# Optimization experiments

Hardware: AMD Instinct MI355X
Metric: run time of the kernel (lower is better)

## Reference

```python
import jax, jax.numpy as jnp
import numpy as np

N_AGENTS = 512
HID = 256
OBS = 128


def setup_inputs() -> dict:
    key = jax.random.key(0)
    ks = jax.random.split(key, 10)
    s = 0.02  # weight init scale
    f32 = jnp.float32
    return {
        "inputs": jax.random.normal(ks[0], (N_AGENTS, OBS), f32),
        "fc1_w": jax.random.normal(ks[1], (HID, OBS), f32) * s,
        "fc1_b": jnp.zeros((HID,), f32),
        "in_proj_w": jax.random.normal(ks[2], (3 * HID, HID), f32) * s,
        "in_proj_b": jnp.zeros((3 * HID,), f32),
        "out_proj_w": jax.random.normal(ks[3], (HID, HID), f32) * s,
        "out_proj_b": jnp.zeros((HID,), f32),
        "fc2_w": jax.random.normal(ks[4], (HID, 2 * HID), f32) * s,
        "fc2_b": jnp.zeros((HID,), f32),
        "fc3_w": jax.random.normal(ks[5], (2, HID), f32) * s,
        "fc3_b": jnp.zeros((2,), f32),
        "vfc2_w": jax.random.normal(ks[6], (HID, HID * N_AGENTS), f32) * s,
        "vfc2_b": jnp.zeros((HID,), f32),
        "vfc3_w": jax.random.normal(ks[7], (1, HID), f32) * s,
        "vfc3_b": jnp.zeros((1,), f32),
    }


def reference(inputs, fc1_w, fc1_b, in_proj_w, in_proj_b, out_proj_w, out_proj_b,
              fc2_w, fc2_b, fc3_w, fc3_b, vfc2_w, vfc2_b, vfc3_w, vfc3_b):
    n = inputs.shape[0]
    d = fc1_w.shape[0]
    # per-agent embed
    hid = jax.nn.relu(inputs @ fc1_w.T + fc1_b)                 # [n, d]
    # single-head self-attention (torch MultiheadAttention, 1 head)
    qkv = hid @ in_proj_w.T + in_proj_b                         # [n, 3d]
    q, k, v = jnp.split(qkv, 3, axis=-1)
    scores = (q @ k.T) / jnp.sqrt(jnp.asarray(d, hid.dtype))    # [n, n]
    attn = jax.nn.softmax(scores, axis=-1)
    h = (attn @ v) @ out_proj_w.T + out_proj_b                  # [n, d]
    # all-pairs edge features restricted to strict upper triangle
    iu0, iu1 = jnp.triu_indices(n, 1)                           # P = n(n-1)/2
    pairs = jnp.concatenate([h[iu0], h[iu1]], axis=1)           # [P, 2d]
    x = jax.nn.relu(pairs @ fc2_w.T + fc2_b)                    # [P, d]
    action_out = jax.nn.softmax(x @ fc3_w.T + fc3_b, axis=-1)   # [P, 2]
    # value head over flattened node embeddings
    vh = jax.nn.relu(hid.reshape(1, -1) @ vfc2_w.T + vfc2_b)    # [1, d]
    value = vh @ vfc3_w.T + vfc3_b                              # [1, 1]
    value = jnp.broadcast_to(value, (action_out.shape[0], 1))   # [P, 1]
    return jnp.concatenate([action_out, value], axis=1)         # [P, 3]
```

## Files before the change

kernel.cpp:

```cpp
#include <hip/hip_runtime.h>
#include <math.h>

#define N_AG   512
#define HIDD   256
#define OBSD   128

__device__ __forceinline__ float dot4(float4 a, float4 b){
    return a.x*b.x + a.y*b.y + a.z*b.z + a.w*b.w;
}

__global__ __launch_bounds__(256) void k_fc1(const float* __restrict__ in,
        const float* __restrict__ w, const float* __restrict__ b,
        float* __restrict__ hid){
    __shared__ float lin[8*OBSD];
    int at = blockIdx.y, ot = blockIdx.x, t = threadIdx.x;
    ((float4*)lin)[t] = ((const float4*)(in + at*8*OBSD))[t];
    __syncthreads();
    int ol = t & 63, g = t >> 6;
    int o = ot*64 + ol;
    const float4* w4 = (const float4*)(w + o*OBSD);
    const float4* la = (const float4*)(lin + (g*2)*OBSD);
    const float4* lb = (const float4*)(lin + (g*2+1)*OBSD);
    float acc0 = 0.f, acc1 = 0.f;
    #pragma unroll
    for (int c = 0; c < OBSD/4; ++c){
        float4 wv = w4[c];
        acc0 += dot4(la[c], wv);
        acc1 += dot4(lb[c], wv);
    }
    float bb = b[o];
    int a0 = at*8 + g*2;
    hid[a0*HIDD + o]     = fmaxf(acc0 + bb, 0.f);
    hid[(a0+1)*HIDD + o] = fmaxf(acc1 + bb, 0.f);
}

__global__ __launch_bounds__(256) void k_qkv(const float* __restrict__ hid,
        const float* __restrict__ w, const float* __restrict__ b,
        float* __restrict__ qkv){
    __shared__ float lin[8*HIDD];
    int at = blockIdx.y, ot = blockIdx.x, t = threadIdx.x;
    const float4* in4 = (const float4*)(hid + at*8*HIDD);
    ((float4*)lin)[t]       = in4[t];
    ((float4*)lin)[t + 256] = in4[t + 256];
    __syncthreads();
    int ol = t & 63, g = t >> 6;
    int o = ot*64 + ol;
    const float4* w4 = (const float4*)(w + o*HIDD);
    const float4* la = (const float4*)(lin + (g*2)*HIDD);
    const float4* lb = (const float4*)(lin + (g*2+1)*HIDD);
    float acc0 = 0.f, acc1 = 0.f;
    #pragma unroll 16
    for (int c = 0; c < HIDD/4; ++c){
        float4 wv = w4[c];
        acc0 += dot4(la[c], wv);
        acc1 += dot4(lb[c], wv);
    }
    float bb = b[o];
    int a0 = at*8 + g*2;
    qkv[a0*768 + o]     = acc0 + bb;
    qkv[(a0+1)*768 + o] = acc1 + bb;
}

__global__ __launch_bounds__(256) void k_attn(const float* __restrict__ qkv,
        const float* __restrict__ ow, const float* __restrict__ ob,
        float* __restrict__ hout){
    __shared__ float q2[2*HIDD];
    __shared__ float sc[2*512];
    __shared__ float av[2*HIDD];
    __shared__ float red[16];
    int r0 = blockIdx.x*2, t = threadIdx.x;
    if (t < 128){
        int r = t >> 6, c4 = t & 63;
        ((float4*)q2)[r*64 + c4] = ((const float4*)(qkv + (r0+r)*768))[c4];
    }
    __syncthreads();
    #pragma unroll
    for (int jj = 0; jj < 2; ++jj){
        int j = t + jj*256;
        const float4* k4 = (const float4*)(qkv + j*768 + HIDD);
        const float4* qa = (const float4*)q2;
        const float4* qb = (const float4*)(q2 + HIDD);
        float a0 = 0.f, a1 = 0.f;
        #pragma unroll 16
        for (int c = 0; c < HIDD/4; ++c){
            float4 kv = k4[c];
            a0 += dot4(qa[c], kv);
            a1 += dot4(qb[c], kv);
        }
        sc[j]       = a0 * 0.0625f;
        sc[512 + j] = a1 * 0.0625f;
    }
    __syncthreads();
    int lane = t & 63, wid = t >> 6;
    float s00 = sc[t], s01 = sc[t+256], s10 = sc[512+t], s11 = sc[512+t+256];
    float m0 = fmaxf(s00, s01), m1 = fmaxf(s10, s11);
    for (int off = 32; off; off >>= 1){
        m0 = fmaxf(m0, __shfl_xor(m0, off));
        m1 = fmaxf(m1, __shfl_xor(m1, off));
    }
    if (lane == 0){ red[wid] = m0; red[4+wid] = m1; }
    __syncthreads();
    m0 = fmaxf(fmaxf(red[0],red[1]), fmaxf(red[2],red[3]));
    m1 = fmaxf(fmaxf(red[4],red[5]), fmaxf(red[6],red[7]));
    float e00 = expf(s00-m0), e01 = expf(s01-m0), e10 = expf(s10-m1), e11 = expf(s11-m1);
    float t0 = e00+e01, t1 = e10+e11;
    for (int off = 32; off; off >>= 1){ t0 += __shfl_xor(t0, off); t1 += __shfl_xor(t1, off); }
    if (lane == 0){ red[8+wid] = t0; red[12+wid] = t1; }
    __syncthreads();
    float inv0 = 1.f/(red[8]+red[9]+red[10]+red[11]);
    float inv1 = 1.f/(red[12]+red[13]+red[14]+red[15]);
    sc[t] = e00*inv0; sc[t+256] = e01*inv0;
    sc[512+t] = e10*inv1; sc[512+t+256] = e11*inv1;
    __syncthreads();
    {
        float acc0 = 0.f, acc1 = 0.f;
        for (int j = 0; j < 512; ++j){
            float vv = qkv[j*768 + 512 + t];
            acc0 += sc[j]*vv;
            acc1 += sc[512+j]*vv;
        }
        av[t] = acc0; av[HIDD+t] = acc1;
    }
    __syncthreads();
    {
        const float4* w4 = (const float4*)(ow + t*HIDD);
        const float4* a4 = (const float4*)av;
        const float4* b4 = (const float4*)(av + HIDD);
        float h0 = 0.f, h1 = 0.f;
        #pragma unroll 16
        for (int c = 0; c < HIDD/4; ++c){
            float4 wv = w4[c];
            h0 += dot4(a4[c], wv);
            h1 += dot4(b4[c], wv);
        }
        float bb = ob[t];
        hout[r0*HIDD + t]     = h0 + bb;
        hout[(r0+1)*HIDD + t] = h1 + bb;
    }
}

__global__ __launch_bounds__(256) void k_ab(const float* __restrict__ hin,
        const float* __restrict__ w, const float* __restrict__ b,
        float* __restrict__ A, float* __restrict__ B){
    __shared__ float lin[8*HIDD];
    int at = blockIdx.y, ot = blockIdx.x, t = threadIdx.x;
    const float4* in4 = (const float4*)(hin + at*8*HIDD);
    ((float4*)lin)[t]       = in4[t];
    ((float4*)lin)[t + 256] = in4[t + 256];
    __syncthreads();
    int ol = t & 63, g = t >> 6;
    int o2 = ot*64 + ol;
    bool isA = o2 < HIDD;
    int o = isA ? o2 : o2 - HIDD;
    const float4* w4 = (const float4*)(w + o*512 + (isA ? 0 : HIDD));
    const float4* la = (const float4*)(lin + (g*2)*HIDD);
    const float4* lb = (const float4*)(lin + (g*2+1)*HIDD);
    float acc0 = 0.f, acc1 = 0.f;
    #pragma unroll 16
    for (int c = 0; c < HIDD/4; ++c){
        float4 wv = w4[c];
        acc0 += dot4(la[c], wv);
        acc1 += dot4(lb[c], wv);
    }
    int a0 = at*8 + g*2;
    float* dst = isA ? A : B;
    float bb = isA ? b[o] : 0.f;
    dst[a0*HIDD + o]     = acc0 + bb;
    dst[(a0+1)*HIDD + o] = acc1 + bb;
}

__global__ __launch_bounds__(256) void k_vpart(const float* __restrict__ hid,
        const float* __restrict__ vw, float* __restrict__ partial){
    int chunk = blockIdx.x, o = blockIdx.y, t = threadIdx.x;
    const float4* h4 = (const float4*)hid;
    const float4* w4 = (const float4*)vw;
    long base  = (long)chunk*4096;
    long wbase = (long)o*32768 + base;
    float acc = 0.f;
    #pragma unroll 4
    for (int it = 0; it < 16; ++it){
        acc += dot4(h4[base + it*256 + t], w4[wbase + it*256 + t]);
    }
    for (int off = 32; off; off >>= 1) acc += __shfl_xor(acc, off);
    __shared__ float red[4];
    int lane = t & 63, wid = t >> 6;
    if (lane == 0) red[wid] = acc;
    __syncthreads();
    if (t == 0) partial[o*8 + chunk] = red[0]+red[1]+red[2]+red[3];
}

__global__ __launch_bounds__(256) void k_value(const float* __restrict__ partial,
        const float* __restrict__ vb, const float* __restrict__ v3w,
        const float* __restrict__ v3b, float* __restrict__ value){
    int t = threadIdx.x;
    float s = vb[t];
    #pragma unroll
    for (int c = 0; c < 8; ++c) s += partial[t*8 + c];
    s = fmaxf(s, 0.f);
    float p = s * v3w[t];
    for (int off = 32; off; off >>= 1) p += __shfl_xor(p, off);
    __shared__ float red[4];
    int lane = t & 63, wid = t >> 6;
    if (lane == 0) red[wid] = p;
    __syncthreads();
    if (t == 0) value[0] = red[0]+red[1]+red[2]+red[3] + v3b[0];
}

__global__ __launch_bounds__(256) void k_pairs(const float* __restrict__ A,
        const float* __restrict__ B, const float* __restrict__ w3,
        const float* __restrict__ b3, const float* __restrict__ value,
        float* __restrict__ out){
    int ti = blockIdx.x, tj = blockIdx.y;
    if (tj < ti) return;
    __shared__ float la[16*260], lb[16*260], lw[256];
    int t = threadIdx.x;
    #pragma unroll
    for (int l = 0; l < 4; ++l){
        int idx = l*256 + t;
        int r = idx >> 6, c4 = idx & 63;
        ((float4*)la)[r*65 + c4] = ((const float4*)A)[(ti*16 + r)*64 + c4];
        ((float4*)lb)[r*65 + c4] = ((const float4*)B)[(tj*16 + r)*64 + c4];
    }
    lw[t] = w3[t] - w3[256 + t];
    __syncthreads();
    float val = value[0];
    float bd  = b3[0] - b3[1];
    int il = t >> 4, jl = t & 15;
    int i = ti*16 + il, j = tj*16 + jl;
    if (j > i){
        const float4* a4 = (const float4*)(la + il*260);
        const float4* b4 = (const float4*)(lb + jl*260);
        const float4* w4 = (const float4*)lw;
        float acc = 0.f;
        #pragma unroll 8
        for (int c = 0; c < 64; ++c){
            float4 aa = a4[c], bb = b4[c], wv = w4[c];
            acc += fmaxf(aa.x + bb.x, 0.f)*wv.x
                 + fmaxf(aa.y + bb.y, 0.f)*wv.y
                 + fmaxf(aa.z + bb.z, 0.f)*wv.z
                 + fmaxf(aa.w + bb.w, 0.f)*wv.w;
        }
        float z = acc + bd;
        float o0 = 1.f/(1.f + expf(-z));
        int p = i*511 - (i*(i-1))/2 + (j - i - 1);
        out[3*p]   = o0;
        out[3*p+1] = 1.f - o0;
        out[3*p+2] = val;
    }
}

extern "C" void kernel_launch(void* const* d_in, const int* in_sizes, int n_in,
                              void* d_out, int out_size, void* d_ws, size_t ws_size,
                              hipStream_t stream){
    const float* inputs = (const float*)d_in[0];
    const float* fc1_w  = (const float*)d_in[1];
    const float* fc1_b  = (const float*)d_in[2];
    const float* inp_w  = (const float*)d_in[3];
    const float* inp_b  = (const float*)d_in[4];
    const float* outp_w = (const float*)d_in[5];
    const float* outp_b = (const float*)d_in[6];
    const float* fc2_w  = (const float*)d_in[7];
    const float* fc2_b  = (const float*)d_in[8];
    const float* fc3_w  = (const float*)d_in[9];
    const float* fc3_b  = (const float*)d_in[10];
    const float* vfc2_w = (const float*)d_in[11];
    const float* vfc2_b = (const float*)d_in[12];
    const float* vfc3_w = (const float*)d_in[13];
    const float* vfc3_b = (const float*)d_in[14];
    float* out = (float*)d_out;
    float* ws  = (float*)d_ws;
    float* hid     = ws;
    float* qkv     = ws + 131072;
    float* h       = ws + 524288;
    float* A       = ws + 655360;
    float* B       = ws + 786432;
    float* partial = ws + 917504;
    float* value   = ws + 919552;

    k_fc1  <<<dim3(4, 64),  256, 0, stream>>>(inputs, fc1_w, fc1_b, hid);
    k_qkv  <<<dim3(12, 64), 256, 0, stream>>>(hid, inp_w, inp_b, qkv);
    k_attn <<<dim3(256),    256, 0, stream>>>(qkv, outp_w, outp_b, h);
    k_ab   <<<dim3(8, 64),  256, 0, stream>>>(h, fc2_w, fc2_b, A, B);
    k_vpart<<<dim3(8, 256), 256, 0, stream>>>(hid, vfc2_w, partial);
    k_value<<<1,            256, 0, stream>>>(partial, vfc2_b, vfc3_w, vfc3_b, value);
    k_pairs<<<dim3(32, 32), 256, 0, stream>>>(A, B, fc3_w, fc3_b, value, out);
}
```

Baseline: 335.3 us.

## Fuse kernels into four launches and split dot-product accumulators

Merges fc1 and the QKV projection into one embed kernel, and runs the value-head partial reduction as extra blocks inside the attention launch. The final value reduction is folded into the A/B projection kernel. Attention now handles one row per block, so there are twice as many blocks, and all dot products use four independent accumulators to shorten the dependency chain. This cuts the launch count from seven to four and overlaps the independent value-head work with attention. In exchange, attention reuses each loaded K/V row across fewer query rows, and the embed kernel has only 128 blocks, each doing more serial work.

New measurement: 435.1 us. 1.3x slower.

```diff
diff --git a/kernel.cpp b/kernel.cpp
--- a/kernel.cpp
+++ b/kernel.cpp
@@ -5,145 +5,138 @@
 #define HIDD   256
 #define OBSD   128
 
-__device__ __forceinline__ float dot4(float4 a, float4 b){
-    return a.x*b.x + a.y*b.y + a.z*b.z + a.w*b.w;
-}
-
-__global__ __launch_bounds__(256) void k_fc1(const float* __restrict__ in,
-        const float* __restrict__ w, const float* __restrict__ b,
-        float* __restrict__ hid){
-    __shared__ float lin[8*OBSD];
-    int at = blockIdx.y, ot = blockIdx.x, t = threadIdx.x;
-    ((float4*)lin)[t] = ((const float4*)(in + at*8*OBSD))[t];
+__device__ __forceinline__ void fma4(float4& acc, float4 a, float4 b){
+    acc.x += a.x*b.x; acc.y += a.y*b.y; acc.z += a.z*b.z; acc.w += a.w*b.w;
+}
+__device__ __forceinline__ float hsum(float4 a){ return (a.x+a.y)+(a.z+a.w); }
+
+__global__ __launch_bounds__(256) void k_embed(const float* __restrict__ in,
+        const float* __restrict__ w1, const float* __restrict__ b1,
+        const float* __restrict__ wq, const float* __restrict__ bq,
+        float* __restrict__ hid, float* __restrict__ qkv){
+    __shared__ float lin[4*OBSD];
+    __shared__ float lh[4*HIDD];
+    int at = blockIdx.x, t = threadIdx.x;
+    if (t < 128) ((float4*)lin)[t] = ((const float4*)(in + at*4*OBSD))[t];
     __syncthreads();
     int ol = t & 63, g = t >> 6;
-    int o = ot*64 + ol;
-    const float4* w4 = (const float4*)(w + o*OBSD);
-    const float4* la = (const float4*)(lin + (g*2)*OBSD);
-    const float4* lb = (const float4*)(lin + (g*2+1)*OBSD);
-    float acc0 = 0.f, acc1 = 0.f;
+    const float4* x4 = (const float4*)(lin + g*OBSD);
     #pragma unroll
-    for (int c = 0; c < OBSD/4; ++c){
-        float4 wv = w4[c];
-        acc0 += dot4(la[c], wv);
-        acc1 += dot4(lb[c], wv);
-    }
-    float bb = b[o];
-    int a0 = at*8 + g*2;
-    hid[a0*HIDD + o]     = fmaxf(acc0 + bb, 0.f);
-    hid[(a0+1)*HIDD + o] = fmaxf(acc1 + bb, 0.f);
-}
-
-__global__ __launch_bounds__(256) void k_qkv(const float* __restrict__ hid,
-        const float* __restrict__ w, const float* __restrict__ b,
-        float* __restrict__ qkv){
-    __shared__ float lin[8*HIDD];
-    int at = blockIdx.y, ot = blockIdx.x, t = threadIdx.x;
-    const float4* in4 = (const float4*)(hid + at*8*HIDD);
-    ((float4*)lin)[t]       = in4[t];
-    ((float4*)lin)[t + 256] = in4[t + 256];
-    __syncthreads();
-    int ol = t & 63, g = t >> 6;
-    int o = ot*64 + ol;
-    const float4* w4 = (const float4*)(w + o*HIDD);
-    const float4* la = (const float4*)(lin + (g*2)*HIDD);
-    const float4* lb = (const float4*)(lin + (g*2+1)*HIDD);
-    float acc0 = 0.f, acc1 = 0.f;
-    #pragma unroll 16
-    for (int c = 0; c < HIDD/4; ++c){
-        float4 wv = w4[c];
-        acc0 += dot4(la[c], wv);
-        acc1 += dot4(lb[c], wv);
-    }
-    float bb = b[o];
-    int a0 = at*8 + g*2;
-    qkv[a0*768 + o]     = acc0 + bb;
-    qkv[(a0+1)*768 + o] = acc1 + bb;
-}
-
-__global__ __launch_bounds__(256) void k_attn(const float* __restrict__ qkv,
+    for (int ot = 0; ot < 4; ++ot){
+        int o = ot*64 + ol;
+        const float4* w4 = (const float4*)(w1 + o*OBSD);
+        float4 acc = {0,0,0,0};
+        #pragma unroll
+        for (int c = 0; c < OBSD/4; ++c) fma4(acc, x4[c], w4[c]);
+        float h = fmaxf(hsum(acc) + b1[o], 0.f);
+        lh[g*HIDD + o] = h;
+        hid[(at*4+g)*HIDD + o] = h;
+    }
+    __syncthreads();
+    const float4* h4 = (const float4*)(lh + g*HIDD);
+    #pragma unroll 2
+    for (int ot = 0; ot < 12; ++ot){
+        int o = ot*64 + ol;
+        const float4* w4 = (const float4*)(wq + o*HIDD);
+        float4 acc = {0,0,0,0};
+        #pragma unroll 16
+        for (int c = 0; c < HIDD/4; ++c) fma4(acc, h4[c], w4[c]);
+        qkv[(at*4+g)*768 + o] = hsum(acc) + bq[o];
+    }
+}
+
+__global__ __launch_bounds__(256) void k_attn_vpart(const float* __restrict__ qkv,
         const float* __restrict__ ow, const float* __restrict__ ob,
-        float* __restrict__ hout){
-    __shared__ float q2[2*HIDD];
-    __shared__ float sc[2*512];
-    __shared__ float av[2*HIDD];
-    __shared__ float red[16];
-    int r0 = blockIdx.x*2, t = threadIdx.x;
-    if (t < 128){
-        int r = t >> 6, c4 = t & 63;
-        ((float4*)q2)[r*64 + c4] = ((const float4*)(qkv + (r0+r)*768))[c4];
-    }
-    __syncthreads();
+        const float* __restrict__ hid, const float* __restrict__ vw,
+        float* __restrict__ hout, float* __restrict__ partial){
+    int t = threadIdx.x;
+    if (blockIdx.x >= N_AG){
+        int id = blockIdx.x - N_AG;
+        int chunk = id & 7, o = id >> 3;
+        const float4* h4 = (const float4*)hid;
+        const float4* w4 = (const float4*)vw;
+        long base  = (long)chunk*4096;
+        long wbase = (long)o*32768 + base;
+        float4 acc4 = {0,0,0,0};
+        #pragma unroll 4
+        for (int it = 0; it < 16; ++it)
+            fma4(acc4, h4[base + it*256 + t], w4[wbase + it*256 + t]);
+        float acc = hsum(acc4);
+        for (int off = 32; off; off >>= 1) acc += __shfl_xor(acc, off);
+        __shared__ float redv[4];
+        int lane = t & 63, wid = t >> 6;
+        if (lane == 0) redv[wid] = acc;
+        __syncthreads();
+        if (t == 0) partial[o*8 + chunk] = redv[0]+redv[1]+redv[2]+redv[3];
+        return;
+    }
+    int r = blockIdx.x;
+    __shared__ float q[HIDD];
+    __shared__ float sc[512];
+    __shared__ float av[HIDD];
+    __shared__ float red2[8];
+    if (t < 64) ((float4*)q)[t] = ((const float4*)(qkv + r*768))[t];
+    __syncthreads();
+    const float4* q4 = (const float4*)q;
     #pragma unroll
     for (int jj = 0; jj < 2; ++jj){
         int j = t + jj*256;
         const float4* k4 = (const float4*)(qkv + j*768 + HIDD);
-        const float4* qa = (const float4*)q2;
-        const float4* qb = (const float4*)(q2 + HIDD);
-        float a0 = 0.f, a1 = 0.f;
+        float4 acc = {0,0,0,0};
         #pragma unroll 16
-        for (int c = 0; c < HIDD/4; ++c){
-            float4 kv = k4[c];
-            a0 += dot4(qa[c], kv);
-            a1 += dot4(qb[c], kv);
-        }
-        sc[j]       = a0 * 0.0625f;
-        sc[512 + j] = a1 * 0.0625f;
+        for (int c = 0; c < HIDD/4; ++c) fma4(acc, q4[c], k4[c]);
+        sc[j] = hsum(acc) * 0.0625f;
     }
     __syncthreads();
     int lane = t & 63, wid = t >> 6;
-    float s00 = sc[t], s01 = sc[t+256], s10 = sc[512+t], s11 = sc[512+t+256];
-    float m0 = fmaxf(s00, s01), m1 = fmaxf(s10, s11);
-    for (int off = 32; off; off >>= 1){
-        m0 = fmaxf(m0, __shfl_xor(m0, off));
-        m1 = fmaxf(m1, __shfl_xor(m1, off));
-    }
-    if (lane == 0){ red[wid] = m0; red[4+wid] = m1; }
-    __syncthreads();
-    m0 = fmaxf(fmaxf(red[0],red[1]), fmaxf(red[2],red[3]));
-    m1 = fmaxf(fmaxf(red[4],red[5]), fmaxf(red[6],red[7]));
-    float e00 = expf(s00-m0), e01 = expf(s01-m0), e10 = expf(s10-m1), e11 = expf(s11-m1);
-    float t0 = e00+e01, t1 = e10+e11;
-    for (int off = 32; off; off >>= 1){ t0 += __shfl_xor(t0, off); t1 += __shfl_xor(t1, off); }
-    if (lane == 0){ red[8+wid] = t0; red[12+wid] = t1; }
-    __syncthreads();
-    float inv0 = 1.f/(red[8]+red[9]+red[10]+red[11]);
-    float inv1 = 1.f/(red[12]+red[13]+red[14]+red[15]);
-    sc[t] = e00*inv0; sc[t+256] = e01*inv0;
-    sc[512+t] = e10*inv1; sc[512+t+256] = e11*inv1;
-    __syncthreads();
-    {
-        float acc0 = 0.f, acc1 = 0.f;
-        for (int j = 0; j < 512; ++j){
-            float vv = qkv[j*768 + 512 + t];
-            acc0 += sc[j]*vv;
-            acc1 += sc[512+j]*vv;
-        }
-        av[t] = acc0; av[HIDD+t] = acc1;
-    }
-    __syncthreads();
-    {
-        const float4* w4 = (const float4*)(ow + t*HIDD);
-        const float4* a4 = (const float4*)av;
-        const float4* b4 = (const float4*)(av + HIDD);
-        float h0 = 0.f, h1 = 0.f;
-        #pragma unroll 16
-        for (int c = 0; c < HIDD/4; ++c){
-            float4 wv = w4[c];
-            h0 += dot4(a4[c], wv);
-            h1 += dot4(b4[c], wv);
-        }
-        float bb = ob[t];
-        hout[r0*HIDD + t]     = h0 + bb;
-        hout[(r0+1)*HIDD + t] = h1 + bb;
-    }
-}
-
-__global__ __launch_bounds__(256) void k_ab(const float* __restrict__ hin,
-        const float* __restrict__ w, const float* __restrict__ b,
-        float* __restrict__ A, float* __restrict__ B){
+    float s0 = sc[t], s1 = sc[t+256];
+    float m = fmaxf(s0, s1);
+    for (int off = 32; off; off >>= 1) m = fmaxf(m, __shfl_xor(m, off));
+    if (lane == 0) red2[wid] = m;
+    __syncthreads();
+    m = fmaxf(fmaxf(red2[0],red2[1]), fmaxf(red2[2],red2[3]));
+    float e0 = expf(s0-m), e1 = expf(s1-m);
+    float s = e0 + e1;
+    for (int off = 32; off; off >>= 1) s += __shfl_xor(s, off);
+    if (lane == 0) red2[4+wid] = s;
+    __syncthreads();
+    float inv = 1.f/(red2[4]+red2[5]+red2[6]+red2[7]);
+    sc[t] = e0*inv; sc[t+256] = e1*inv;
+    __syncthreads();
+    float acc = 0.f;
+    #pragma unroll 8
+    for (int j = 0; j < 512; ++j) acc += sc[j]*qkv[j*768 + 512 + t];
+    av[t] = acc;
+    __syncthreads();
+    const float4* a4 = (const float4*)av;
+    const float4* w4 = (const float4*)(ow + t*HIDD);
+    float4 acc4 = {0,0,0,0};
+    #pragma unroll 16
+    for (int c = 0; c < HIDD/4; ++c) fma4(acc4, a4[c], w4[c]);
+    hout[r*HIDD + t] = hsum(acc4) + ob[t];
+}
+
+__global__ __launch_bounds__(256) void k_ab_value(const float* __restrict__ hin,
+        const float* __restrict__ w2, const float* __restrict__ b2,
+        const float* __restrict__ partial, const float* __restrict__ vb,
+        const float* __restrict__ v3w, const float* __restrict__ v3b,
+        float* __restrict__ A, float* __restrict__ B, float* __restrict__ value){
+    int t = threadIdx.x;
+    if (blockIdx.x == 512){
+        float s = vb[t];
+        #pragma unroll
+        for (int c = 0; c < 8; ++c) s += partial[t*8 + c];
+        s = fmaxf(s, 0.f) * v3w[t];
+        for (int off = 32; off; off >>= 1) s += __shfl_xor(s, off);
+        __shared__ float redv[4];
+        int lane = t & 63, wid = t >> 6;
+        if (lane == 0) redv[wid] = s;
+        __syncthreads();
+        if (t == 0) value[0] = redv[0]+redv[1]+redv[2]+redv[3] + v3b[0];
+        return;
+    }
     __shared__ float lin[8*HIDD];
-    int at = blockIdx.y, ot = blockIdx.x, t = threadIdx.x;
+    int id = blockIdx.x, at = id >> 3, ot = id & 7;
     const float4* in4 = (const float4*)(hin + at*8*HIDD);
     ((float4*)lin)[t]       = in4[t];
     ((float4*)lin)[t + 256] = in4[t + 256];
@@ -152,58 +145,21 @@
     int o2 = ot*64 + ol;
     bool isA = o2 < HIDD;
     int o = isA ? o2 : o2 - HIDD;
-    const float4* w4 = (const float4*)(w + o*512 + (isA ? 0 : HIDD));
+    const float4* w4 = (const float4*)(w2 + o*512 + (isA ? 0 : HIDD));
     const float4* la = (const float4*)(lin + (g*2)*HIDD);
     const float4* lb = (const float4*)(lin + (g*2+1)*HIDD);
-    float acc0 = 0.f, acc1 = 0.f;
+    float4 acc0 = {0,0,0,0}, acc1 = {0,0,0,0};
     #pragma unroll 16
     for (int c = 0; c < HIDD/4; ++c){
         float4 wv = w4[c];
-        acc0 += dot4(la[c], wv);
-        acc1 += dot4(lb[c], wv);
+        fma4(acc0, la[c], wv);
+        fma4(acc1, lb[c], wv);
     }
     int a0 = at*8 + g*2;
     float* dst = isA ? A : B;
-    float bb = isA ? b[o] : 0.f;
-    dst[a0*HIDD + o]     = acc0 + bb;
-    dst[(a0+1)*HIDD + o] = acc1 + bb;
-}
-
-__global__ __launch_bounds__(256) void k_vpart(const float* __restrict__ hid,
-        const float* __restrict__ vw, float* __restrict__ partial){
-    int chunk = blockIdx.x, o = blockIdx.y, t = threadIdx.x;
-    const float4* h4 = (const float4*)hid;
-    const float4* w4 = (const float4*)vw;
-    long base  = (long)chunk*4096;
-    long wbase = (long)o*32768 + base;
-    float acc = 0.f;
-    #pragma unroll 4
-    for (int it = 0; it < 16; ++it){
-        acc += dot4(h4[base + it*256 + t], w4[wbase + it*256 + t]);
-    }
-    for (int off = 32; off; off >>= 1) acc += __shfl_xor(acc, off);
-    __shared__ float red[4];
-    int lane = t & 63, wid = t >> 6;
-    if (lane == 0) red[wid] = acc;
-    __syncthreads();
-    if (t == 0) partial[o*8 + chunk] = red[0]+red[1]+red[2]+red[3];
-}
-
-__global__ __launch_bounds__(256) void k_value(const float* __restrict__ partial,
-        const float* __restrict__ vb, const float* __restrict__ v3w,
-        const float* __restrict__ v3b, float* __restrict__ value){
-    int t = threadIdx.x;
-    float s = vb[t];
-    #pragma unroll
-    for (int c = 0; c < 8; ++c) s += partial[t*8 + c];
-    s = fmaxf(s, 0.f);
-    float p = s * v3w[t];
-    for (int off = 32; off; off >>= 1) p += __shfl_xor(p, off);
-    __shared__ float red[4];
-    int lane = t & 63, wid = t >> 6;
-    if (lane == 0) red[wid] = p;
-    __syncthreads();
-    if (t == 0) value[0] = red[0]+red[1]+red[2]+red[3] + v3b[0];
+    float bb = isA ? b2[o] : 0.f;
+    dst[a0*HIDD + o]     = hsum(acc0) + bb;
+    dst[(a0+1)*HIDD + o] = hsum(acc1) + bb;
 }
 
 __global__ __launch_bounds__(256) void k_pairs(const float* __restrict__ A,
@@ -231,16 +187,16 @@
         const float4* a4 = (const float4*)(la + il*260);
         const float4* b4 = (const float4*)(lb + jl*260);
         const float4* w4 = (const float4*)lw;
-        float acc = 0.f;
+        float4 acc = {0,0,0,0};
         #pragma unroll 8
         for (int c = 0; c < 64; ++c){
             float4 aa = a4[c], bb = b4[c], wv = w4[c];
-            acc += fmaxf(aa.x + bb.x, 0.f)*wv.x
-                 + fmaxf(aa.y + bb.y, 0.f)*wv.y
-                 + fmaxf(aa.z + bb.z, 0.f)*wv.z
-                 + fmaxf(aa.w + bb.w, 0.f)*wv.w;
+            acc.x += fmaxf(aa.x + bb.x, 0.f)*wv.x;
+            acc.y += fmaxf(aa.y + bb.y, 0.f)*wv.y;
+            acc.z += fmaxf(aa.z + bb.z, 0.f)*wv.z;
+            acc.w += fmaxf(aa.w + bb.w, 0.f)*wv.w;
         }
-        float z = acc + bd;
+        float z = hsum(acc) + bd;
         float o0 = 1.f/(1.f + expf(-z));
         int p = i*511 - (i*(i-1))/2 + (j - i - 1);
         out[3*p]   = o0;
@@ -277,11 +233,8 @@
     float* partial = ws + 917504;
     float* value   = ws + 919552;
 
-    k_fc1  <<<dim3(4, 64),  256, 0, stream>>>(inputs, fc1_w, fc1_b, hid);
-    k_qkv  <<<dim3(12, 64), 256, 0, stream>>>(hid, inp_w, inp_b, qkv);
-    k_attn <<<dim3(256),    256, 0, stream>>>(qkv, outp_w, outp_b, h);
-    k_ab   <<<dim3(8, 64),  256, 0, stream>>>(h, fc2_w, fc2_b, A, B);
-    k_vpart<<<dim3(8, 256), 256, 0, stream>>>(hid, vfc2_w, partial);
-    k_value<<<1,            256, 0, stream>>>(partial, vfc2_b, vfc3_w, vfc3_b, value);
-    k_pairs<<<dim3(32, 32), 256, 0, stream>>>(A, B, fc3_w, fc3_b, value, out);
-}
+    k_embed     <<<dim3(128),       256, 0, stream>>>(inputs, fc1_w, fc1_b, inp_w, inp_b, hid, qkv);
+    k_attn_vpart<<<dim3(2560),      256, 0, stream>>>(qkv, outp_w, outp_b, hid, vfc2_w, h, partial);
+    k_ab_value  <<<dim3(513),       256, 0, stream>>>(h, fc2_w, fc2_b, partial, vfc2_b, vfc3_w, vfc3_b, A, B, value);
+    k_pairs     <<<dim3(32, 32),    256, 0, stream>>>(A, B, fc3_w, fc3_b, value, out);
+}
```

## Merge value-head kernels into attention and fc2 launches; use vector accumulators

Applied to the files above, without the earlier changes.

The value-head partial reduction now runs as extra blocks inside the attention kernel, and the final value reduction runs as an extra block of the fc2 A/B kernel. This cuts the launch count from seven to five and lets the memory-bound value-head weight stream overlap with the attention blocks. Dot-product loops also switch to four independent float4 accumulators to break the serial FMA dependency chain, and the attention V loop gets an unroll pragma. The cost is more register pressure and slightly different floating-point summation order.

Result: faster. 314.2 us (-6.3%).

```diff
diff --git a/kernel.cpp b/kernel.cpp
--- a/kernel.cpp
+++ b/kernel.cpp
@@ -5,9 +5,10 @@
 #define HIDD   256
 #define OBSD   128
 
-__device__ __forceinline__ float dot4(float4 a, float4 b){
-    return a.x*b.x + a.y*b.y + a.z*b.z + a.w*b.w;
-}
+__device__ __forceinline__ void fma4(float4& acc, float4 a, float4 b){
+    acc.x += a.x*b.x; acc.y += a.y*b.y; acc.z += a.z*b.z; acc.w += a.w*b.w;
+}
+__device__ __forceinline__ float hsum(float4 a){ return (a.x+a.y)+(a.z+a.w); }
 
 __global__ __launch_bounds__(256) void k_fc1(const float* __restrict__ in,
         const float* __restrict__ w, const float* __restrict__ b,
@@ -21,17 +22,17 @@
     const float4* w4 = (const float4*)(w + o*OBSD);
     const float4* la = (const float4*)(lin + (g*2)*OBSD);
     const float4* lb = (const float4*)(lin + (g*2+1)*OBSD);
-    float acc0 = 0.f, acc1 = 0.f;
+    float4 a0 = {0,0,0,0}, a1 = {0,0,0,0};
     #pragma unroll
     for (int c = 0; c < OBSD/4; ++c){
         float4 wv = w4[c];
-        acc0 += dot4(la[c], wv);
-        acc1 += dot4(lb[c], wv);
+        fma4(a0, la[c], wv);
+        fma4(a1, lb[c], wv);
     }
     float bb = b[o];
-    int a0 = at*8 + g*2;
-    hid[a0*HIDD + o]     = fmaxf(acc0 + bb, 0.f);
-    hid[(a0+1)*HIDD + o] = fmaxf(acc1 + bb, 0.f);
+    int ag = at*8 + g*2;
+    hid[ag*HIDD + o]     = fmaxf(hsum(a0) + bb, 0.f);
+    hid[(ag+1)*HIDD + o] = fmaxf(hsum(a1) + bb, 0.f);
 }
 
 __global__ __launch_bounds__(256) void k_qkv(const float* __restrict__ hid,
@@ -48,47 +49,69 @@
     const float4* w4 = (const float4*)(w + o*HIDD);
     const float4* la = (const float4*)(lin + (g*2)*HIDD);
     const float4* lb = (const float4*)(lin + (g*2+1)*HIDD);
-    float acc0 = 0.f, acc1 = 0.f;
+    float4 a0 = {0,0,0,0}, a1 = {0,0,0,0};
     #pragma unroll 16
     for (int c = 0; c < HIDD/4; ++c){
         float4 wv = w4[c];
-        acc0 += dot4(la[c], wv);
-        acc1 += dot4(lb[c], wv);
+        fma4(a0, la[c], wv);
+        fma4(a1, lb[c], wv);
     }
     float bb = b[o];
-    int a0 = at*8 + g*2;
-    qkv[a0*768 + o]     = acc0 + bb;
-    qkv[(a0+1)*768 + o] = acc1 + bb;
-}
-
-__global__ __launch_bounds__(256) void k_attn(const float* __restrict__ qkv,
+    int ag = at*8 + g*2;
+    qkv[ag*768 + o]     = hsum(a0) + bb;
+    qkv[(ag+1)*768 + o] = hsum(a1) + bb;
+}
+
+__global__ __launch_bounds__(256) void k_attn_vpart(const float* __restrict__ qkv,
         const float* __restrict__ ow, const float* __restrict__ ob,
-        float* __restrict__ hout){
+        const float* __restrict__ hid, const float* __restrict__ vw,
+        float* __restrict__ hout, float* __restrict__ partial){
+    int t = threadIdx.x;
+    if (blockIdx.x >= 256){
+        int id = blockIdx.x - 256;
+        int chunk = id & 7, o = id >> 3;
+        const float4* h4 = (const float4*)hid;
+        const float4* w4 = (const float4*)vw;
+        long base  = (long)chunk*4096;
+        long wbase = (long)o*32768 + base;
+        float4 acc4 = {0,0,0,0};
+        #pragma unroll 4
+        for (int it = 0; it < 16; ++it)
+            fma4(acc4, h4[base + it*256 + t], w4[wbase + it*256 + t]);
+        float acc = hsum(acc4);
+        for (int off = 32; off; off >>= 1) acc += __shfl_xor(acc, off);
+        __shared__ float redv[4];
+        int lane = t & 63, wid = t >> 6;
+        if (lane == 0) redv[wid] = acc;
+        __syncthreads();
+        if (t == 0) partial[o*8 + chunk] = redv[0]+redv[1]+redv[2]+redv[3];
+        return;
+    }
+    int r0 = blockIdx.x*2;
     __shared__ float q2[2*HIDD];
     __shared__ float sc[2*512];
     __shared__ float av[2*HIDD];
     __shared__ float red[16];
-    int r0 = blockIdx.x*2, t = threadIdx.x;
     if (t < 128){
         int r = t >> 6, c4 = t & 63;
         ((float4*)q2)[r*64 + c4] = ((const float4*)(qkv + (r0+r)*768))[c4];
     }
     __syncthreads();
+    const float4* qa = (const float4*)q2;
+    const float4* qb = (const float4*)(q2 + HIDD);
     #pragma unroll
     for (int jj = 0; jj < 2; ++jj){
         int j = t + jj*256;
         const float4* k4 = (const float4*)(qkv + j*768 + HIDD);
-        const float4* qa = (const float4*)q2;
-        const float4* qb = (const float4*)(q2 + HIDD);
-        float a0 = 0.f, a1 = 0.f;
+        float4 acc0 = {0,0,0,0}, acc1 = {0,0,0,0};
         #pragma unroll 16
         for (int c = 0; c < HIDD/4; ++c){
             float4 kv = k4[c];
-            a0 += dot4(qa[c], kv);
-            a1 += dot4(qb[c], kv);
-        }
-        sc[j]       = a0 * 0.0625f;
-        sc[512 + j] = a1 * 0.0625f;
+            fma4(acc0, qa[c], kv);
+            fma4(acc1, qb[c], kv);
+        }
+        sc[j]       = hsum(acc0) * 0.0625f;
+        sc[512 + j] = hsum(acc1) * 0.0625f;
     }
     __syncthreads();
     int lane = t & 63, wid = t >> 6;
@@ -114,6 +137,7 @@
     __syncthreads();
     {
         float acc0 = 0.f, acc1 = 0.f;
+        #pragma unroll 8
         for (int j = 0; j < 512; ++j){
             float vv = qkv[j*768 + 512 + t];
             acc0 += sc[j]*vv;
@@ -126,24 +150,40 @@
         const float4* w4 = (const float4*)(ow + t*HIDD);
         const float4* a4 = (const float4*)av;
         const float4* b4 = (const float4*)(av + HIDD);
-        float h0 = 0.f, h1 = 0.f;
+        float4 h0 = {0,0,0,0}, h1 = {0,0,0,0};
         #pragma unroll 16
         for (int c = 0; c < HIDD/4; ++c){
             float4 wv = w4[c];
-            h0 += dot4(a4[c], wv);
-            h1 += dot4(b4[c], wv);
+            fma4(h0, a4[c], wv);
+            fma4(h1, b4[c], wv);
         }
         float bb = ob[t];
-        hout[r0*HIDD + t]     = h0 + bb;
-        hout[(r0+1)*HIDD + t] = h1 + bb;
-    }
-}
-
-__global__ __launch_bounds__(256) void k_ab(const float* __restrict__ hin,
-        const float* __restrict__ w, const float* __restrict__ b,
-        float* __restrict__ A, float* __restrict__ B){
+        hout[r0*HIDD + t]     = hsum(h0) + bb;
+        hout[(r0+1)*HIDD + t] = hsum(h1) + bb;
+    }
+}
+
+__global__ __launch_bounds__(256) void k_ab_value(const float* __restrict__ hin,
+        const float* __restrict__ w2, const float* __restrict__ b2,
+        const float* __restrict__ partial, const float* __restrict__ vb,
+        const float* __restrict__ v3w, const float* __restrict__ v3b,
+        float* __restrict__ A, float* __restrict__ B, float* __restrict__ value){
+    int t = threadIdx.x;
+    if (blockIdx.x == 512){
+        float s = vb[t];
+        #pragma unroll
+        for (int c = 0; c < 8; ++c) s += partial[t*8 + c];
+        s = fmaxf(s, 0.f) * v3w[t];
+        for (int off = 32; off; off >>= 1) s += __shfl_xor(s, off);
+        __shared__ float redv[4];
+        int lane = t & 63, wid = t >> 6;
+        if (lane == 0) redv[wid] = s;
+        __syncthreads();
+        if (t == 0) value[0] = redv[0]+redv[1]+redv[2]+redv[3] + v3b[0];
+        return;
+    }
     __shared__ float lin[8*HIDD];
-    int at = blockIdx.y, ot = blockIdx.x, t = threadIdx.x;
+    int id = blockIdx.x, at = id >> 3, ot = id & 7;
     const float4* in4 = (const float4*)(hin + at*8*HIDD);
     ((float4*)lin)[t]       = in4[t];
     ((float4*)lin)[t + 256] = in4[t + 256];
@@ -152,58 +192,21 @@
     int o2 = ot*64 + ol;
     bool isA = o2 < HIDD;
     int o = isA ? o2 : o2 - HIDD;
-    const float4* w4 = (const float4*)(w + o*512 + (isA ? 0 : HIDD));
+    const float4* w4 = (const float4*)(w2 + o*512 + (isA ? 0 : HIDD));
     const float4* la = (const float4*)(lin + (g*2)*HIDD);
     const float4* lb = (const float4*)(lin + (g*2+1)*HIDD);
-    float acc0 = 0.f, acc1 = 0.f;
+    float4 acc0 = {0,0,0,0}, acc1 = {0,0,0,0};
     #pragma unroll 16
     for (int c = 0; c < HIDD/4; ++c){
         float4 wv = w4[c];
-        acc0 += dot4(la[c], wv);
-        acc1 += dot4(lb[c], wv);
+        fma4(acc0, la[c], wv);
+        fma4(acc1, lb[c], wv);
     }
     int a0 = at*8 + g*2;
     float* dst = isA ? A : B;
-    float bb = isA ? b[o] : 0.f;
-    dst[a0*HIDD + o]     = acc0 + bb;
-    dst[(a0+1)*HIDD + o] = acc1 + bb;
-}
-
-__global__ __launch_bounds__(256) void k_vpart(const float* __restrict__ hid,
-        const float* __restrict__ vw, float* __restrict__ partial){
-    int chunk = blockIdx.x, o = blockIdx.y, t = threadIdx.x;
-    const float4* h4 = (const float4*)hid;
-    const float4* w4 = (const float4*)vw;
-    long base  = (long)chunk*4096;
-    long wbase = (long)o*32768 + base;
-    float acc = 0.f;
-    #pragma unroll 4
-    for (int it = 0; it < 16; ++it){
-        acc += dot4(h4[base + it*256 + t], w4[wbase + it*256 + t]);
-    }
-    for (int off = 32; off; off >>= 1) acc += __shfl_xor(acc, off);
-    __shared__ float red[4];
-    int lane = t & 63, wid = t >> 6;
-    if (lane == 0) red[wid] = acc;
-    __syncthreads();
-    if (t == 0) partial[o*8 + chunk] = red[0]+red[1]+red[2]+red[3];
-}
-
-__global__ __launch_bounds__(256) void k_value(const float* __restrict__ partial,
-        const float* __restrict__ vb, const float* __restrict__ v3w,
-        const float* __restrict__ v3b, float* __restrict__ value){
-    int t = threadIdx.x;
-    float s = vb[t];
-    #pragma unroll
-    for (int c = 0; c < 8; ++c) s += partial[t*8 + c];
-    s = fmaxf(s, 0.f);
-    float p = s * v3w[t];
-    for (int off = 32; off; off >>= 1) p += __shfl_xor(p, off);
-    __shared__ float red[4];
-    int lane = t & 63, wid = t >> 6;
-    if (lane == 0) red[wid] = p;
-    __syncthreads();
-    if (t == 0) value[0] = red[0]+red[1]+red[2]+red[3] + v3b[0];
+    float bb = isA ? b2[o] : 0.f;
+    dst[a0*HIDD + o]     = hsum(acc0) + bb;
+    dst[(a0+1)*HIDD + o] = hsum(acc1) + bb;
 }
 
 __global__ __launch_bounds__(256) void k_pairs(const float* __restrict__ A,
@@ -231,16 +234,16 @@
         const float4* a4 = (const float4*)(la + il*260);
         const float4* b4 = (const float4*)(lb + jl*260);
         const float4* w4 = (const float4*)lw;
-        float acc = 0.f;
+        float4 acc = {0,0,0,0};
         #pragma unroll 8
         for (int c = 0; c < 64; ++c){
             float4 aa = a4[c], bb = b4[c], wv = w4[c];
-            acc += fmaxf(aa.x + bb.x, 0.f)*wv.x
-                 + fmaxf(aa.y + bb.y, 0.f)*wv.y
-                 + fmaxf(aa.z + bb.z, 0.f)*wv.z
-                 + fmaxf(aa.w + bb.w, 0.f)*wv.w;
-        }
-        float z = acc + bd;
+            acc.x += fmaxf(aa.x + bb.x, 0.f)*wv.x;
+            acc.y += fmaxf(aa.y + bb.y, 0.f)*wv.y;
+            acc.z += fmaxf(aa.z + bb.z, 0.f)*wv.z;
+            acc.w += fmaxf(aa.w + bb.w, 0.f)*wv.w;
+        }
+        float z = hsum(acc) + bd;
         float o0 = 1.f/(1.f + expf(-z));
         int p = i*511 - (i*(i-1))/2 + (j - i - 1);
         out[3*p]   = o0;
@@ -277,11 +280,9 @@
     float* partial = ws + 917504;
     float* value   = ws + 919552;
 
-    k_fc1  <<<dim3(4, 64),  256, 0, stream>>>(inputs, fc1_w, fc1_b, hid);
-    k_qkv  <<<dim3(12, 64), 256, 0, stream>>>(hid, inp_w, inp_b, qkv);
-    k_attn <<<dim3(256),    256, 0, stream>>>(qkv, outp_w, outp_b, h);
-    k_ab   <<<dim3(8, 64),  256, 0, stream>>>(h, fc2_w, fc2_b, A, B);
-    k_vpart<<<dim3(8, 256), 256, 0, stream>>>(hid, vfc2_w, partial);
-    k_value<<<1,            256, 0, stream>>>(partial, vfc2_b, vfc3_w, vfc3_b, value);
-    k_pairs<<<dim3(32, 32), 256, 0, stream>>>(A, B, fc3_w, fc3_b, value, out);
-}
+    k_fc1       <<<dim3(4, 64),  256, 0, stream>>>(inputs, fc1_w, fc1_b, hid);
+    k_qkv       <<<dim3(12, 64), 256, 0, stream>>>(hid, inp_w, inp_b, qkv);
+    k_attn_vpart<<<dim3(2304),   256, 0, stream>>>(qkv, outp_w, outp_b, hid, vfc2_w, h, partial);
+    k_ab_value  <<<dim3(513),    256, 0, stream>>>(h, fc2_w, fc2_b, partial, vfc2_b, vfc3_w, vfc3_b, A, B, value);
+    k_pairs     <<<dim3(32, 32), 256, 0, stream>>>(A, B, fc3_w, fc3_b, value, out);
+}
```
